# Kernel optimization log

Measured on AMD Instinct MI355X. Metric: run time of the kernel, lower is better.

## Reference

```python
import jax, jax.numpy as jnp
import numpy as np

PNUM = 128
BATCH = 8192


def setup_inputs() -> dict:
    key = jax.random.key(0)
    k0, k1, k2 = jax.random.split(key, 3)
    return {
        "pred0": jax.random.normal(k0, (BATCH, PNUM, 2), dtype=jnp.float32),
        "pred1": jax.random.normal(k1, (BATCH, PNUM, 2), dtype=jnp.float32),
        "gt": jax.random.normal(k2, (BATCH, PNUM, 2), dtype=jnp.float32),
    }


def _smooth_l1(d):
    # F.smooth_l1_loss with default beta=1.0, reduction='none'
    a = jnp.abs(d)
    return jnp.where(a < 1.0, 0.5 * d * d, a - 0.5)


def _match_loss(pred, gt):
    # pred, gt: [B, pnum, 2]
    pnum = pred.shape[1]
    # cyclic index: idx[i, j] = (i + j) % pnum  (row i = gt rolled by i)
    idx = (jnp.arange(pnum)[:, None] + jnp.arange(pnum)[None, :]) % pnum
    gt_expand = gt[:, idx]                      # [B, pnum, pnum, 2]
    diff = pred[:, None, :, :] - gt_expand      # broadcast pred over shift dim i
    dis = _smooth_l1(diff).sum(-1).mean(axis=2)  # [B, pnum] mean over vertices j
    return jnp.min(dis, axis=1)                  # min over cyclic shift i -> [B]


def reference(pred0, pred1, gt):
    loss = _match_loss(pred0, gt).mean() + _match_loss(pred1, gt).mean()
    return loss / 2.0
```

## Files before the change

### kernel.cpp

```cpp
#include <hip/hip_runtime.h>

#define PNUM 128
#define BATCH 8192
#define WPB 4
#define GRID1 (BATCH / WPB)

typedef _Float16 h2 __attribute__((ext_vector_type(2)));
typedef _Float16 h4 __attribute__((ext_vector_type(4)));

__device__ __forceinline__ h2 cvt2(float x, float y) {
    return __builtin_bit_cast(h2, __builtin_amdgcn_cvt_pkrtz(x, y));
}

__device__ __forceinline__ void unit(h2 p, h2 q, float& acc) {
    h2 d = p - q;
    h2 a = __builtin_bit_cast(h2, __builtin_bit_cast(unsigned, d) & 0x7fff7fffu);
    h2 m = __builtin_elementwise_min(a, (h2)(_Float16)1.0f);
    h2 t = __builtin_elementwise_fma(m, (h2)(_Float16)-0.5f, a);
    acc = __builtin_amdgcn_fdot2(m, t, acc, false);
}

__device__ __forceinline__ h2 lo2(h4 v) { return __builtin_shufflevector(v, v, 0, 1); }
__device__ __forceinline__ h2 hi2(h4 v) { return __builtin_shufflevector(v, v, 2, 3); }

__device__ __forceinline__ h2 bcast(unsigned v, int lane) {
    return __builtin_bit_cast(h2, __builtin_amdgcn_readlane((int)v, lane));
}

__global__ __launch_bounds__(64 * WPB, 6) void match_fused(
        const float* __restrict__ pred0,
        const float* __restrict__ pred1,
        const float* __restrict__ gt,
        float* __restrict__ out) {
    __shared__ __align__(16) h4 ring[WPB][128];

    const int t = threadIdx.x;
    const int k = t & 63;
    const int w = __builtin_amdgcn_readfirstlane(t >> 6);
    const int b = blockIdx.x * WPB + w;

    h4* ring4 = ring[w];

    const float4* gv4 = (const float4*)(gt    + (size_t)b * (PNUM * 2));
    const float4* p0v = (const float4*)(pred0 + (size_t)b * (PNUM * 2));
    const float4* p1v = (const float4*)(pred1 + (size_t)b * (PNUM * 2));
    {
        float4 g = gv4[k];
        h2 c0 = cvt2(g.x, g.y), c1 = cvt2(g.z, g.w);
        h4 gh = {c0.x, c0.y, c1.x, c1.y};
        ring4[k] = gh; ring4[k + 64] = gh;
    }
    uint2 P0u, P1u;
    {
        float4 p = p0v[k];
        P0u.x = __builtin_bit_cast(unsigned, cvt2(p.x, p.y));
        P0u.y = __builtin_bit_cast(unsigned, cvt2(p.z, p.w));
        p = p1v[k];
        P1u.x = __builtin_bit_cast(unsigned, cvt2(p.x, p.y));
        P1u.y = __builtin_bit_cast(unsigned, cvt2(p.z, p.w));
    }

    h4 W = ring4[k];
    float a00 = 0.f, a01 = 0.f, a10 = 0.f, a11 = 0.f;

#pragma unroll 4
    for (int hh = 0; hh < 32; ++hh) {
        h4 na = ring4[k + 2 * hh + 1];
        h4 nb = ring4[k + 2 * hh + 2];

        h2 p0a = bcast(P0u.x, 2 * hh),     p0b = bcast(P0u.y, 2 * hh);
        h2 p0c = bcast(P0u.x, 2 * hh + 1), p0d = bcast(P0u.y, 2 * hh + 1);
        h2 p1a = bcast(P1u.x, 2 * hh),     p1b = bcast(P1u.y, 2 * hh);
        h2 p1c = bcast(P1u.x, 2 * hh + 1), p1d = bcast(P1u.y, 2 * hh + 1);

        h2 Wl = lo2(W), Wh = hi2(W), Al = lo2(na), Ah = hi2(na), Bl = lo2(nb);

        unit(p0a, Wl, a00); unit(p0b, Wh, a00); unit(p0c, Al, a00); unit(p0d, Ah, a00);
        unit(p0a, Wh, a01); unit(p0b, Al, a01); unit(p0c, Ah, a01); unit(p0d, Bl, a01);
        unit(p1a, Wl, a10); unit(p1b, Wh, a10); unit(p1c, Al, a10); unit(p1d, Ah, a10);
        unit(p1a, Wh, a11); unit(p1b, Al, a11); unit(p1c, Ah, a11); unit(p1d, Bl, a11);

        W = nb;
    }

    float r0 = fminf(a00, a01);
    float r1 = fminf(a10, a11);
#pragma unroll
    for (int m = 32; m > 0; m >>= 1) {
        r0 = fminf(r0, __shfl_xor(r0, m, 64));
        r1 = fminf(r1, __shfl_xor(r1, m, 64));
    }

    __shared__ float bsum[WPB];
    if (k == 0) bsum[w] = r0 + r1;
    __syncthreads();
    if (t == 0) {
        float blockpart = bsum[0] + bsum[1] + bsum[2] + bsum[3];
        atomicAdd(out, blockpart * (1.0f / (2.0f * BATCH * PNUM)));
    }
}

extern "C" void kernel_launch(void* const* d_in, const int* in_sizes, int n_in,
                              void* d_out, int out_size, void* d_ws, size_t ws_size,
                              hipStream_t stream) {
    const float* pred0 = (const float*)d_in[0];
    const float* pred1 = (const float*)d_in[1];
    const float* gt    = (const float*)d_in[2];
    float* out = (float*)d_out;

    (void)hipMemsetAsync(out, 0, sizeof(float), stream);
    match_fused<<<GRID1, 64 * WPB, 0, stream>>>(pred0, pred1, gt, out);
}
```

Measured before the change: 124.1 us.

## Process two batches per wave with four shifts per lane and LDS-broadcast preds

Each wave now handles two batch rows (32 lanes each), and every lane evaluates four consecutive cyclic shifts instead of two, so each loaded gt window is reused across more shifts. Pred values are staged in LDS and read as uniform 16-byte broadcast loads instead of being fetched with per-vertex readlane instructions. The grid is halved and the occupancy hint drops from 6 to 4 to fit the extra accumulators and LDS. The cost is more registers and more LDS traffic per lane, which may reduce the number of waves in flight.

```diff
diff --git a/kernel.cpp b/kernel.cpp
--- a/kernel.cpp
+++ b/kernel.cpp
@@ -3,13 +3,18 @@
 #define PNUM 128
 #define BATCH 8192
 #define WPB 4
-#define GRID1 (BATCH / WPB)
+#define GRID1 (BATCH / (2 * WPB))
 
 typedef _Float16 h2 __attribute__((ext_vector_type(2)));
 typedef _Float16 h4 __attribute__((ext_vector_type(4)));
+typedef _Float16 h8 __attribute__((ext_vector_type(8)));
 
 __device__ __forceinline__ h2 cvt2(float x, float y) {
     return __builtin_bit_cast(h2, __builtin_amdgcn_cvt_pkrtz(x, y));
+}
+__device__ __forceinline__ h4 cvt4(float4 v) {
+    h2 a = cvt2(v.x, v.y), b = cvt2(v.z, v.w);
+    return (h4){a.x, a.y, b.x, b.y};
 }
 
 __device__ __forceinline__ void unit(h2 p, h2 q, float& acc) {
@@ -22,77 +27,89 @@
 
 __device__ __forceinline__ h2 lo2(h4 v) { return __builtin_shufflevector(v, v, 0, 1); }
 __device__ __forceinline__ h2 hi2(h4 v) { return __builtin_shufflevector(v, v, 2, 3); }
-
-__device__ __forceinline__ h2 bcast(unsigned v, int lane) {
-    return __builtin_bit_cast(h2, __builtin_amdgcn_readlane((int)v, lane));
+__device__ __forceinline__ h4 lo4(h8 v) { return __builtin_shufflevector(v, v, 0, 1, 2, 3); }
+__device__ __forceinline__ h4 hi4(h8 v) { return __builtin_shufflevector(v, v, 4, 5, 6, 7); }
+__device__ __forceinline__ h2 el2(h8 v, int i) {
+    return (h2){v[2 * i], v[2 * i + 1]};
 }
 
-__global__ __launch_bounds__(64 * WPB, 6) void match_fused(
+__global__ __launch_bounds__(64 * WPB, 4) void match_fused(
         const float* __restrict__ pred0,
         const float* __restrict__ pred1,
         const float* __restrict__ gt,
         float* __restrict__ out) {
-    __shared__ __align__(16) h4 ring[WPB][128];
+    __shared__ __align__(16) h4 ring [WPB][2][128];
+    __shared__ __align__(16) h4 preds[WPB][2][2][64];
 
-    const int t = threadIdx.x;
-    const int k = t & 63;
-    const int w = __builtin_amdgcn_readfirstlane(t >> 6);
-    const int b = blockIdx.x * WPB + w;
+    const int t  = threadIdx.x;
+    const int k  = t & 63;
+    const int w  = __builtin_amdgcn_readfirstlane(t >> 6);
+    const int h  = k >> 5;
+    const int kk = k & 31;
+    const int b  = 2 * (blockIdx.x * WPB + w) + h;
 
-    h4* ring4 = ring[w];
+    h4* ring4 = ring[w][h];
+    h4* q0 = preds[w][h][0];
+    h4* q1 = preds[w][h][1];
 
     const float4* gv4 = (const float4*)(gt    + (size_t)b * (PNUM * 2));
     const float4* p0v = (const float4*)(pred0 + (size_t)b * (PNUM * 2));
     const float4* p1v = (const float4*)(pred1 + (size_t)b * (PNUM * 2));
     {
-        float4 g = gv4[k];
-        h2 c0 = cvt2(g.x, g.y), c1 = cvt2(g.z, g.w);
-        h4 gh = {c0.x, c0.y, c1.x, c1.y};
-        ring4[k] = gh; ring4[k + 64] = gh;
-    }
-    uint2 P0u, P1u;
-    {
-        float4 p = p0v[k];
-        P0u.x = __builtin_bit_cast(unsigned, cvt2(p.x, p.y));
-        P0u.y = __builtin_bit_cast(unsigned, cvt2(p.z, p.w));
-        p = p1v[k];
-        P1u.x = __builtin_bit_cast(unsigned, cvt2(p.x, p.y));
-        P1u.y = __builtin_bit_cast(unsigned, cvt2(p.z, p.w));
+        h4 v = cvt4(gv4[kk]);      ring4[kk]      = v; ring4[kk + 64] = v;
+        v    = cvt4(gv4[kk + 32]); ring4[kk + 32] = v; ring4[kk + 96] = v;
+        q0[kk]      = cvt4(p0v[kk]);
+        q0[kk + 32] = cvt4(p0v[kk + 32]);
+        q1[kk]      = cvt4(p1v[kk]);
+        q1[kk + 32] = cvt4(p1v[kk + 32]);
     }
 
-    h4 W = ring4[k];
-    float a00 = 0.f, a01 = 0.f, a10 = 0.f, a11 = 0.f;
+    const h8* q0_8 = (const h8*)q0;
+    const h8* q1_8 = (const h8*)q1;
+
+    h8 wi = *(const h8*)&ring4[2 * kk];
+    h4 w0 = lo4(wi), w1 = hi4(wi);
+
+    float r00 = 0.f, r01 = 0.f, r02 = 0.f, r03 = 0.f;
+    float r10 = 0.f, r11 = 0.f, r12 = 0.f, r13 = 0.f;
 
 #pragma unroll 4
     for (int hh = 0; hh < 32; ++hh) {
-        h4 na = ring4[k + 2 * hh + 1];
-        h4 nb = ring4[k + 2 * hh + 2];
+        h8 n  = *(const h8*)&ring4[2 * kk + 2 * hh + 2];
+        h8 P0 = q0_8[hh];
+        h8 P1 = q1_8[hh];
+        h4 w2 = lo4(n), w3 = hi4(n);
 
-        h2 p0a = bcast(P0u.x, 2 * hh),     p0b = bcast(P0u.y, 2 * hh);
-        h2 p0c = bcast(P0u.x, 2 * hh + 1), p0d = bcast(P0u.y, 2 * hh + 1);
-        h2 p1a = bcast(P1u.x, 2 * hh),     p1b = bcast(P1u.y, 2 * hh);
-        h2 p1c = bcast(P1u.x, 2 * hh + 1), p1d = bcast(P1u.y, 2 * hh + 1);
+        h2 A0 = lo2(w0), A1 = hi2(w0), A2 = lo2(w1), A3 = hi2(w1);
+        h2 A4 = lo2(w2), A5 = hi2(w2), A6 = lo2(w3);
+        h2 p0a = el2(P0, 0), p0b = el2(P0, 1), p0c = el2(P0, 2), p0d = el2(P0, 3);
+        h2 p1a = el2(P1, 0), p1b = el2(P1, 1), p1c = el2(P1, 2), p1d = el2(P1, 3);
 
-        h2 Wl = lo2(W), Wh = hi2(W), Al = lo2(na), Ah = hi2(na), Bl = lo2(nb);
+        unit(p0a, A0, r00); unit(p0b, A1, r00); unit(p0c, A2, r00); unit(p0d, A3, r00);
+        unit(p0a, A1, r01); unit(p0b, A2, r01); unit(p0c, A3, r01); unit(p0d, A4, r01);
+        unit(p0a, A2, r02); unit(p0b, A3, r02); unit(p0c, A4, r02); unit(p0d, A5, r02);
+        unit(p0a, A3, r03); unit(p0b, A4, r03); unit(p0c, A5, r03); unit(p0d, A6, r03);
 
-        unit(p0a, Wl, a00); unit(p0b, Wh, a00); unit(p0c, Al, a00); unit(p0d, Ah, a00);
-        unit(p0a, Wh, a01); unit(p0b, Al, a01); unit(p0c, Ah, a01); unit(p0d, Bl, a01);
-        unit(p1a, Wl, a10); unit(p1b, Wh, a10); unit(p1c, Al, a10); unit(p1d, Ah, a10);
-        unit(p1a, Wh, a11); unit(p1b, Al, a11); unit(p1c, Ah, a11); unit(p1d, Bl, a11);
+        unit(p1a, A0, r10); unit(p1b, A1, r10); unit(p1c, A2, r10); unit(p1d, A3, r10);
+        unit(p1a, A1, r11); unit(p1b, A2, r11); unit(p1c, A3, r11); unit(p1d, A4, r11);
+        unit(p1a, A2, r12); unit(p1b, A3, r12); unit(p1c, A4, r12); unit(p1d, A5, r12);
+        unit(p1a, A3, r13); unit(p1b, A4, r13); unit(p1c, A5, r13); unit(p1d, A6, r13);
 
-        W = nb;
+        w0 = w2; w1 = w3;
     }
 
-    float r0 = fminf(a00, a01);
-    float r1 = fminf(a10, a11);
+    float m0 = fminf(fminf(r00, r01), fminf(r02, r03));
+    float m1 = fminf(fminf(r10, r11), fminf(r12, r13));
 #pragma unroll
-    for (int m = 32; m > 0; m >>= 1) {
-        r0 = fminf(r0, __shfl_xor(r0, m, 64));
-        r1 = fminf(r1, __shfl_xor(r1, m, 64));
+    for (int m = 16; m > 0; m >>= 1) {
+        m0 = fminf(m0, __shfl_xor(m0, m, 64));
+        m1 = fminf(m1, __shfl_xor(m1, m, 64));
     }
+    float s = m0 + m1;
+    s += __shfl_xor(s, 32, 64);
 
     __shared__ float bsum[WPB];
-    if (k == 0) bsum[w] = r0 + r1;
+    if (k == 0) bsum[w] = s;
     __syncthreads();
     if (t == 0) {
         float blockpart = bsum[0] + bsum[1] + bsum[2] + bsum[3];
```

New measurement: 116.6 us. -6.0%, faster.
